# Kernel optimization log

Hardware: AMD Instinct MI355X
Metric: run time of the kernel (lower is better)

The kernel has to match this reference:

```python
import jax, jax.numpy as jnp
import numpy as np

E = 1024
H = 16
CH = E // H

def setup_inputs() -> dict:
    key = jax.random.key(0)
    ks = jax.random.split(key, 9)
    s = E ** -0.5
    return {
        'x': jax.random.normal(ks[0], (4, 2048, E), dtype=jnp.float32),
        'Wq': jax.random.normal(ks[1], (E, E), dtype=jnp.float32) * s,
        'bq': jnp.zeros((E,), dtype=jnp.float32),
        'Wk': jax.random.normal(ks[2], (E, E), dtype=jnp.float32) * s,
        'bk': jnp.zeros((E,), dtype=jnp.float32),
        'Wv': jax.random.normal(ks[3], (E, E), dtype=jnp.float32) * s,
        'bv': jnp.zeros((E,), dtype=jnp.float32),
        'Wo': jax.random.normal(ks[4], (E, E), dtype=jnp.float32) * s,
        'bo': jnp.zeros((E,), dtype=jnp.float32),
    }

def _split_heads(t):
    # [..., n, H*ch] -> [..., H, n, ch]
    b, n, e = t.shape
    return t.reshape(b, n, H, CH).transpose(0, 2, 1, 3)

def reference(x, Wq, bq, Wk, bk, Wv, bv, Wo, bo):
    scale = CH ** -0.5
    q = _split_heads(x @ Wq.T + bq)  # [b,H,n,ch]
    k = _split_heads(x @ Wk.T + bk)
    v = _split_heads(x @ Wv.T + bv)
    att = jnp.einsum('bhqc,bhkc->bhqk', q, k) * scale
    att = jax.nn.softmax(att, axis=-1)
    out = jnp.einsum('bhqk,bhkc->bhqc', att, v)  # [b,H,n,ch]
    b, h, n, c = out.shape
    out = out.transpose(0, 2, 1, 3).reshape(b, n, h * c)
    return out @ Wo.T + bo
```

## Files before the change

kernel.cpp:

```cpp
#include <hip/hip_runtime.h>
#include <stdint.h>

#define EMB   1024
#define NHEAD 16
#define CHD   64
#define NB    4
#define SEQ   2048
#define NTOK  (NB * SEQ)
#define KDIM  1024

typedef __attribute__((ext_vector_type(8))) short  bf16x8;
typedef __attribute__((ext_vector_type(4))) short  short4v;
typedef __attribute__((ext_vector_type(4))) float  f32x4;
typedef __attribute__((ext_vector_type(4))) float  float4v;

__device__ __forceinline__ short f2bf(float f) {
    unsigned int u = __float_as_uint(f);
    u += 0x7fffu + ((u >> 16) & 1u);
    return (short)(u >> 16);
}

__device__ __forceinline__ void async16(const short* g, short* l) {
    __builtin_amdgcn_global_load_lds((__attribute__((address_space(1))) void const*)g,
                                     (__attribute__((address_space(3))) void*)l, 16, 0, 0);
}

__global__ __launch_bounds__(256) void cvt_all(const float* __restrict__ x,
                                               const float* __restrict__ Wq,
                                               const float* __restrict__ Wk,
                                               const float* __restrict__ Wv,
                                               const float* __restrict__ Wo,
                                               short* __restrict__ xb,
                                               short* __restrict__ Wqb,
                                               short* __restrict__ Wkb,
                                               short* __restrict__ Wvb,
                                               short* __restrict__ Wob) {
    int bid = blockIdx.x;
    const float* src;
    short* dst;
    int idx;
    if (bid < 8192) {
        src = x; dst = xb; idx = bid * 256 + threadIdx.x;
    } else {
        int w  = (bid - 8192) >> 10;
        int lb = (bid - 8192) & 1023;
        src = (w == 0) ? Wq : (w == 1) ? Wk : (w == 2) ? Wv : Wo;
        dst = (w == 0) ? Wqb : (w == 1) ? Wkb : (w == 2) ? Wvb : Wob;
        idx = lb * 256 + threadIdx.x;
    }
    float4v v = ((const float4v*)src)[idx];
    short4v s;
    s.x = f2bf(v.x); s.y = f2bf(v.y); s.z = f2bf(v.z); s.w = f2bf(v.w);
    ((short4v*)dst)[idx] = s;
}

__device__ __forceinline__ void gemm_core(const short* __restrict__ Atile,
                                          const short* __restrict__ Btile,
                                          short* As, short* Bs, f32x4 acc[4][4]) {
    const int tid  = threadIdx.x;
    const int wave = tid >> 6, lane = tid & 63;
    const int quad = lane >> 4, l16 = lane & 15;
    const int wm = (wave >> 1) * 64, wn = (wave & 1) * 64;
    const int srow = lane >> 2;
    const int scol = (lane & 3) * 8;

    for (int k0 = 0; k0 < KDIM; k0 += 32) {
        __syncthreads();
#pragma unroll
        for (int c = 0; c < 2; ++c) {
            int chunk = wave * 2 + c;
            int row = chunk * 16 + srow;
            async16(Atile + (size_t)row * KDIM + k0 + scol, As + chunk * 512);
            async16(Btile + (size_t)row * KDIM + k0 + scol, Bs + chunk * 512);
        }
        __syncthreads();
        bf16x8 af[4], bfr[4];
#pragma unroll
        for (int i = 0; i < 4; ++i)
            af[i] = *(const bf16x8*)&As[(wm + i * 16 + l16) * 32 + quad * 8];
#pragma unroll
        for (int j = 0; j < 4; ++j)
            bfr[j] = *(const bf16x8*)&Bs[(wn + j * 16 + l16) * 32 + quad * 8];
#pragma unroll
        for (int i = 0; i < 4; ++i)
#pragma unroll
            for (int j = 0; j < 4; ++j)
                acc[i][j] = __builtin_amdgcn_mfma_f32_16x16x32_bf16(af[i], bfr[j], acc[i][j], 0, 0, 0);
    }
}

#define QSCALE 0.1803368801111204f
__global__ __launch_bounds__(256) void qkv_gemm(const short* __restrict__ xb,
                                                const short* __restrict__ Wqb,
                                                const short* __restrict__ Wkb,
                                                const short* __restrict__ Wvb,
                                                const float* __restrict__ bq,
                                                const float* __restrict__ bk,
                                                const float* __restrict__ bv,
                                                short* __restrict__ Qb,
                                                short* __restrict__ Kb,
                                                short* __restrict__ Vtb) {
    __shared__ short As[128 * 32], Bs[128 * 32];
    const int bm = blockIdx.x, bn = blockIdx.y;
    const int which = bn >> 3;
    const int ew = (bn & 7) * 128;
    const short* W    = (which == 0) ? Wqb : (which == 1) ? Wkb : Wvb;
    const float* bias = (which == 0) ? bq  : (which == 1) ? bk  : bv;
    const float sc    = (which == 0) ? QSCALE : 1.0f;

    const short* Xt = xb + (size_t)bm * 128 * KDIM;
    const short* Wt = W + (size_t)ew * KDIM;
    const short* Ap = (which == 2) ? Wt : Xt;
    const short* Bp = (which == 2) ? Xt : Wt;

    f32x4 acc[4][4];
    const f32x4 z = {0.f, 0.f, 0.f, 0.f};
#pragma unroll
    for (int i = 0; i < 4; ++i)
#pragma unroll
        for (int j = 0; j < 4; ++j) acc[i][j] = z;

    gemm_core(Ap, Bp, As, Bs, acc);

    const int lane = threadIdx.x & 63, wave = threadIdx.x >> 6;
    const int quad = lane >> 4, l16 = lane & 15;
    const int wm = (wave >> 1) * 64, wn = (wave & 1) * 64;

    if (which == 2) {
#pragma unroll
        for (int i = 0; i < 4; ++i)
#pragma unroll
            for (int j = 0; j < 4; ++j)
#pragma unroll
                for (int r = 0; r < 4; ++r) {
                    int e = ew + wm + i * 16 + quad * 4 + r;
                    int token = bm * 128 + wn + j * 16 + l16;
                    int bb = token >> 11, nn = token & 2047;
                    int hh = e >> 6, cc = e & 63;
                    Vtb[(((size_t)bb * NHEAD + hh) * CHD + cc) * SEQ + nn] =
                        f2bf(acc[i][j][r] + bias[e]);
                }
    } else {
        short* dst = which ? Kb : Qb;
#pragma unroll
        for (int i = 0; i < 4; ++i)
#pragma unroll
            for (int j = 0; j < 4; ++j)
#pragma unroll
                for (int r = 0; r < 4; ++r) {
                    int token = bm * 128 + wm + i * 16 + quad * 4 + r;
                    int bb = token >> 11, nn = token & 2047;
                    int e = ew + wn + j * 16 + l16;
                    int hh = e >> 6, cc = e & 63;
                    dst[(((size_t)bb * NHEAD + hh) * SEQ + nn) * CHD + cc] =
                        f2bf((acc[i][j][r] + bias[e]) * sc);
                }
    }
}

__global__ __launch_bounds__(256, 4) void attn(const short* __restrict__ Qb,
                                               const short* __restrict__ Kb,
                                               const short* __restrict__ Vtb,
                                               short* __restrict__ AOb) {
    __shared__ short Ks[16 * 512];
    __shared__ short Vs[16 * 512];

    const int qt = blockIdx.x;
    const int bh = blockIdx.y;
    const int tid = threadIdx.x, wave = tid >> 6, lane = tid & 63;
    const int quad = lane >> 4, l16 = lane & 15;

    const short* Kg = Kb  + (size_t)bh * SEQ * CHD;
    const short* Vg = Vtb + (size_t)bh * CHD * SEQ;

    bf16x8 qf0[2], qf1[2];
#pragma unroll
    for (int g = 0; g < 2; ++g) {
        const short* Qg = Qb + ((size_t)bh * SEQ + qt * 128 + wave * 32 + g * 16 + l16) * CHD;
        qf0[g] = *(const bf16x8*)(Qg + quad * 8);
        qf1[g] = *(const bf16x8*)(Qg + 32 + quad * 8);
    }

    const int kr = lane >> 3, ku = (lane & 7) ^ kr;
    const int vr = lane >> 4, vu = (lane & 15) ^ (vr << 2);

    int koff[4], voff[4];
#pragma unroll
    for (int cc = 0; cc < 4; ++cc) {
        int c = wave * 4 + cc;
        int l = c * 8 + kr;
        int j = l >> 4, m = l & 15;
        int kvg = ((j >> 1) << 5) + ((m >> 2) << 3) + ((j & 1) << 2) + (m & 3);
        koff[cc] = kvg * CHD + ku * 8;
        voff[cc] = (c * 4 + vr) * SEQ + vu * 8;
    }

    const int krow = l16 & 7;
    const int kbase = ((l16 >> 3) * 512) + krow * 64;
    const short* kp0 = Ks + kbase + ((quad ^ krow) << 3);
    const short* kp1 = Ks + kbase + (((4 + quad) ^ krow) << 3);
    const int vrow = l16 & 3;
    const short* vp = Vs + (l16 >> 2) * 512 + vrow * 128 + quad * 8;

    const f32x4 zf = {0.f, 0.f, 0.f, 0.f};
    const bf16x8 onesv = {16256, 16256, 16256, 16256, 16256, 16256, 16256, 16256};
    f32x4 O[2][4];
#pragma unroll
    for (int g = 0; g < 2; ++g)
#pragma unroll
        for (int nb = 0; nb < 4; ++nb) O[g][nb] = zf;
    f32x4 lacc[2];
    lacc[0] = zf; lacc[1] = zf;

    const short* Kgp = Kg;
    const short* Vgp = Vg;

    for (int kt = 0; kt < 16; ++kt) {
        __syncthreads();
#pragma unroll
        for (int cc = 0; cc < 4; ++cc) {
            int c = wave * 4 + cc;
            async16(Kgp + koff[cc], Ks + c * 512);
            async16(Vgp + voff[cc], Vs + c * 512);
        }
        Kgp += 128 * CHD;
        Vgp += 128;
        __syncthreads();

#pragma unroll
        for (int kk = 0; kk < 4; ++kk) {
            bf16x8 kA0 = *(const bf16x8*)(kp0 + (2 * kk) * 1024);
            bf16x8 kA1 = *(const bf16x8*)(kp1 + (2 * kk) * 1024);
            bf16x8 kB0 = *(const bf16x8*)(kp0 + (2 * kk + 1) * 1024);
            bf16x8 kB1 = *(const bf16x8*)(kp1 + (2 * kk + 1) * 1024);

            union { int i[4]; bf16x8 v; } pf[2];
#pragma unroll
            for (int g = 0; g < 2; ++g) {
                f32x4 sA = __builtin_amdgcn_mfma_f32_16x16x32_bf16(kA0, qf0[g], zf, 0, 0, 0);
                sA = __builtin_amdgcn_mfma_f32_16x16x32_bf16(kA1, qf1[g], sA, 0, 0, 0);
                f32x4 sB = __builtin_amdgcn_mfma_f32_16x16x32_bf16(kB0, qf0[g], zf, 0, 0, 0);
                sB = __builtin_amdgcn_mfma_f32_16x16x32_bf16(kB1, qf1[g], sB, 0, 0, 0);

                unsigned a0 = __float_as_uint(__builtin_amdgcn_exp2f(sA.x));
                unsigned a1 = __float_as_uint(__builtin_amdgcn_exp2f(sA.y));
                unsigned a2 = __float_as_uint(__builtin_amdgcn_exp2f(sA.z));
                unsigned a3 = __float_as_uint(__builtin_amdgcn_exp2f(sA.w));
                unsigned b0 = __float_as_uint(__builtin_amdgcn_exp2f(sB.x));
                unsigned b1 = __float_as_uint(__builtin_amdgcn_exp2f(sB.y));
                unsigned b2 = __float_as_uint(__builtin_amdgcn_exp2f(sB.z));
                unsigned b3 = __float_as_uint(__builtin_amdgcn_exp2f(sB.w));
                pf[g].i[0] = __builtin_amdgcn_perm(a1, a0, 0x07060302u);
                pf[g].i[1] = __builtin_amdgcn_perm(a3, a2, 0x07060302u);
                pf[g].i[2] = __builtin_amdgcn_perm(b1, b0, 0x07060302u);
                pf[g].i[3] = __builtin_amdgcn_perm(b3, b2, 0x07060302u);

                lacc[g] = __builtin_amdgcn_mfma_f32_16x16x32_bf16(pf[g].v, onesv, lacc[g], 0, 0, 0);
            }

            const short* vpk = vp + ((kk ^ vrow) << 5);
#pragma unroll
            for (int nb = 0; nb < 4; ++nb) {
                bf16x8 vf = *(const bf16x8*)(vpk + nb * 2048);
#pragma unroll
                for (int g = 0; g < 2; ++g)
                    O[g][nb] = __builtin_amdgcn_mfma_f32_16x16x32_bf16(pf[g].v, vf, O[g][nb], 0, 0, 0);
            }
        }
    }

    const int b = bh >> 4, h = bh & 15;
#pragma unroll
    for (int g = 0; g < 2; ++g) {
        float linv[4];
#pragma unroll
        for (int r = 0; r < 4; ++r) linv[r] = 1.0f / lacc[g][r];
#pragma unroll
        for (int nb = 0; nb < 4; ++nb)
#pragma unroll
            for (int r = 0; r < 4; ++r) {
                int n = qt * 128 + wave * 32 + g * 16 + quad * 4 + r;
                int cc = nb * 16 + l16;
                AOb[((size_t)b * SEQ + n) * EMB + h * CHD + cc] = f2bf(O[g][nb][r] * linv[r]);
            }
    }
}

__global__ __launch_bounds__(256) void out_gemm(const short* __restrict__ AOb,
                                                const short* __restrict__ Wob,
                                                const float* __restrict__ bo,
                                                float* __restrict__ out) {
    __shared__ short As[128 * 32], Bs[128 * 32];
    const int bm = blockIdx.x, bn = blockIdx.y;

    f32x4 acc[4][4];
    const f32x4 z = {0.f, 0.f, 0.f, 0.f};
#pragma unroll
    for (int i = 0; i < 4; ++i)
#pragma unroll
        for (int j = 0; j < 4; ++j) acc[i][j] = z;

    gemm_core(AOb + (size_t)bm * 128 * KDIM, Wob + (size_t)bn * 128 * KDIM, As, Bs, acc);

    const int lane = threadIdx.x & 63, wave = threadIdx.x >> 6;
    const int quad = lane >> 4, l16 = lane & 15;
    const int wm = (wave >> 1) * 64, wn = (wave & 1) * 64;
#pragma unroll
    for (int i = 0; i < 4; ++i)
#pragma unroll
        for (int j = 0; j < 4; ++j)
#pragma unroll
            for (int r = 0; r < 4; ++r) {
                int token = bm * 128 + wm + i * 16 + quad * 4 + r;
                int e = bn * 128 + wn + j * 16 + l16;
                out[(size_t)token * EMB + e] = acc[i][j][r] + bo[e];
            }
}

extern "C" void kernel_launch(void* const* d_in, const int* in_sizes, int n_in,
                              void* d_out, int out_size, void* d_ws, size_t ws_size,
                              hipStream_t stream) {
    const float* x  = (const float*)d_in[0];
    const float* Wq = (const float*)d_in[1];
    const float* bq = (const float*)d_in[2];
    const float* Wk = (const float*)d_in[3];
    const float* bk = (const float*)d_in[4];
    const float* Wv = (const float*)d_in[5];
    const float* bv = (const float*)d_in[6];
    const float* Wo = (const float*)d_in[7];
    const float* bo = (const float*)d_in[8];

    char* ws = (char*)d_ws;
    short* xb  = (short*)(ws + 0);
    short* Wqb = (short*)(ws + (size_t)16 * 1024 * 1024);
    short* Wkb = (short*)(ws + (size_t)18 * 1024 * 1024);
    short* Wvb = (short*)(ws + (size_t)20 * 1024 * 1024);
    short* Wob = (short*)(ws + (size_t)22 * 1024 * 1024);
    short* Qb  = (short*)(ws + (size_t)24 * 1024 * 1024);
    short* Kb  = (short*)(ws + (size_t)40 * 1024 * 1024);
    short* Vtb = (short*)(ws + (size_t)56 * 1024 * 1024);
    short* AOb = (short*)(ws + (size_t)72 * 1024 * 1024);

    cvt_all<<<dim3(8192 + 4096), dim3(256), 0, stream>>>(x, Wq, Wk, Wv, Wo,
                                                         xb, Wqb, Wkb, Wvb, Wob);
    qkv_gemm<<<dim3(64, 24), dim3(256), 0, stream>>>(xb, Wqb, Wkb, Wvb, bq, bk, bv, Qb, Kb, Vtb);
    attn<<<dim3(16, 64), dim3(256), 0, stream>>>(Qb, Kb, Vtb, AOb);
    out_gemm<<<dim3(64, 8), dim3(256), 0, stream>>>(AOb, Wob, bo, (float*)d_out);
}
```

Before: 281.8 us.

## Split QKV projection into pipelined 256x256 Q/K GEMM and separate V kernel

Replaces the combined QKV GEMM with a new 512-thread 256x256-tile GEMM for Q and K, and a separate V projection kernel. The Q/K kernel double-buffers LDS with async global-to-LDS loads, uses XOR-swizzled LDS layout, interleaves MFMA windows with barriers and setprio, and waits on explicit vmcnt. It relies on Wkb sitting directly after Wqb in the workspace so both can be read as one contiguous weight matrix. The goal is higher MFMA utilisation and more data reuse for the bulk of the projection, at the cost of 128KB of dynamic LDS per block and an extra kernel launch.

Result: faster. 262.3 us (-6.9%).

```diff
diff --git a/kernel.cpp b/kernel.cpp
--- a/kernel.cpp
+++ b/kernel.cpp
@@ -90,28 +90,149 @@
 }
 
 #define QSCALE 0.1803368801111204f
-__global__ __launch_bounds__(256) void qkv_gemm(const short* __restrict__ xb,
-                                                const short* __restrict__ Wqb,
-                                                const short* __restrict__ Wkb,
-                                                const short* __restrict__ Wvb,
+
+
+#define MFMA16(A,B,C) __builtin_amdgcn_mfma_f32_16x16x32_bf16(A,B,C,0,0,0)
+#define BARR  { __builtin_amdgcn_s_barrier(); __builtin_amdgcn_sched_barrier(0); }
+#define VMC4  asm volatile("s_waitcnt vmcnt(4)" ::: "memory");
+#define VMC0  asm volatile("s_waitcnt vmcnt(0)" ::: "memory");
+#define PRIO1 __builtin_amdgcn_s_setprio(1);
+#define PRIO0 __builtin_amdgcn_s_setprio(0);
+
+#define STAGE_A_(BUF,H,T) { \
+    async16(aS0 + (size_t)(H)*131072 + (T)*64, sm + (BUF)*32768 + (H)*8192 + stA); \
+    async16(aS1 + (size_t)(H)*131072 + (T)*64, sm + (BUF)*32768 + (H)*8192 + 4096 + stA); }
+#define STAGE_B_(BUF,H,T) { \
+    async16(bS0 + (size_t)(H)*131072 + (T)*64, sm + (BUF)*32768 + 16384 + (H)*8192 + stA); \
+    async16(bS1 + (size_t)(H)*131072 + (T)*64, sm + (BUF)*32768 + 16384 + (H)*8192 + 4096 + stA); }
+
+#define LDB_(BUF) { \
+    const short* _pb = sm + (BUF)*32768 + bro; \
+    bfr[0][0] = *(const bf16x8*)(_pb + ac0);        bfr[0][1] = *(const bf16x8*)(_pb + ac1); \
+    bfr[1][0] = *(const bf16x8*)(_pb + 1024 + ac0); bfr[1][1] = *(const bf16x8*)(_pb + 1024 + ac1); \
+    bfr[2][0] = *(const bf16x8*)(_pb + 2048 + ac0); bfr[2][1] = *(const bf16x8*)(_pb + 2048 + ac1); \
+    bfr[3][0] = *(const bf16x8*)(_pb + 3072 + ac0); bfr[3][1] = *(const bf16x8*)(_pb + 3072 + ac1); }
+
+#define LDA_(BUF,Q) { \
+    const short* _pa = sm + (BUF)*32768 + aro + (Q)*2048; \
+    af[0][0] = *(const bf16x8*)(_pa + ac0);        af[0][1] = *(const bf16x8*)(_pa + ac1); \
+    af[1][0] = *(const bf16x8*)(_pa + 1024 + ac0); af[1][1] = *(const bf16x8*)(_pa + 1024 + ac1); }
+
+#define MF_(Q) { \
+    acc[2*(Q)][0]   = MFMA16(af[0][0], bfr[0][0], acc[2*(Q)][0]); \
+    acc[2*(Q)][0]   = MFMA16(af[0][1], bfr[0][1], acc[2*(Q)][0]); \
+    acc[2*(Q)][1]   = MFMA16(af[0][0], bfr[1][0], acc[2*(Q)][1]); \
+    acc[2*(Q)][1]   = MFMA16(af[0][1], bfr[1][1], acc[2*(Q)][1]); \
+    acc[2*(Q)][2]   = MFMA16(af[0][0], bfr[2][0], acc[2*(Q)][2]); \
+    acc[2*(Q)][2]   = MFMA16(af[0][1], bfr[2][1], acc[2*(Q)][2]); \
+    acc[2*(Q)][3]   = MFMA16(af[0][0], bfr[3][0], acc[2*(Q)][3]); \
+    acc[2*(Q)][3]   = MFMA16(af[0][1], bfr[3][1], acc[2*(Q)][3]); \
+    acc[2*(Q)+1][0] = MFMA16(af[1][0], bfr[0][0], acc[2*(Q)+1][0]); \
+    acc[2*(Q)+1][0] = MFMA16(af[1][1], bfr[0][1], acc[2*(Q)+1][0]); \
+    acc[2*(Q)+1][1] = MFMA16(af[1][0], bfr[1][0], acc[2*(Q)+1][1]); \
+    acc[2*(Q)+1][1] = MFMA16(af[1][1], bfr[1][1], acc[2*(Q)+1][1]); \
+    acc[2*(Q)+1][2] = MFMA16(af[1][0], bfr[2][0], acc[2*(Q)+1][2]); \
+    acc[2*(Q)+1][2] = MFMA16(af[1][1], bfr[2][1], acc[2*(Q)+1][2]); \
+    acc[2*(Q)+1][3] = MFMA16(af[1][0], bfr[3][0], acc[2*(Q)+1][3]); \
+    acc[2*(Q)+1][3] = MFMA16(af[1][1], bfr[3][1], acc[2*(Q)+1][3]); }
+
+#define WINDOW(RB, AB, TA, BB, TB) \
+    LDB_(RB) LDA_(RB,0) STAGE_A_(AB,0,TA) BARR \
+    PRIO1 MF_(0) PRIO0 BARR \
+    LDA_(RB,1) STAGE_A_(AB,1,TA) BARR \
+    PRIO1 MF_(1) PRIO0 BARR \
+    LDA_(RB,2) STAGE_B_(BB,0,TB) BARR \
+    PRIO1 MF_(2) PRIO0 BARR \
+    LDA_(RB,3) STAGE_B_(BB,1,TB) BARR \
+    PRIO1 MF_(3) PRIO0 VMC4 BARR
+
+__global__ __launch_bounds__(512, 2) void qk256(const short* __restrict__ xb,
+                                                const short* __restrict__ Wqk,
                                                 const float* __restrict__ bq,
                                                 const float* __restrict__ bk,
-                                                const float* __restrict__ bv,
                                                 short* __restrict__ Qb,
-                                                short* __restrict__ Kb,
-                                                short* __restrict__ Vtb) {
+                                                short* __restrict__ Kb) {
+    extern __shared__ short sm[];
+    const int bm = blockIdx.x, bn = blockIdx.y;
+    const int tid = threadIdx.x;
+    const int w = tid >> 6, lane = tid & 63;
+    const int kq = lane >> 4, l16 = lane & 15;
+    const int wmi = w >> 2, wni = w & 3;
+
+    const int colsw = ((lane & 7) * 8) ^ (((lane >> 5) & 1) << 4);
+    const short* aS0 = xb  + (size_t)(bm * 256 + w * 8 + (lane >> 3)) * 1024 + colsw;
+    const short* aS1 = aS0 + (size_t)64 * 1024;
+    const short* bS0 = Wqk + (size_t)(bn * 256 + w * 8 + (lane >> 3)) * 1024 + colsw;
+    const short* bS1 = bS0 + (size_t)64 * 1024;
+    const int stA = w * 512;
+
+    const int swz = (l16 & 4) ? 16 : 0;
+    const int ac0 = (kq * 8) ^ swz;
+    const int ac1 = (32 + kq * 8) ^ swz;
+    const int aro = wmi * 8192 + l16 * 64;
+    const int bro = 16384 + (wni >> 1) * 8192 + ((wni & 1) * 64 + l16) * 64;
+
+    f32x4 acc[8][4];
+    const f32x4 z = {0.f, 0.f, 0.f, 0.f};
+#pragma unroll
+    for (int m = 0; m < 8; ++m)
+#pragma unroll
+        for (int n = 0; n < 4; ++n) acc[m][n] = z;
+    bf16x8 bfr[4][2], af[2][2];
+
+    STAGE_A_(0,0,0) STAGE_A_(0,1,0) STAGE_B_(0,0,0) STAGE_B_(0,1,0)
+    STAGE_B_(1,0,1) STAGE_B_(1,1,1)
+    VMC4 BARR
+
+    for (int it = 0; it < 7; ++it) {
+        const int te = 2 * it;
+        WINDOW(0, 1, te + 1, 0, te + 2)
+        WINDOW(1, 0, te + 2, 1, te + 3)
+    }
+    LDB_(0) LDA_(0,0) STAGE_A_(1,0,15) BARR
+    PRIO1 MF_(0) PRIO0 BARR
+    LDA_(0,1) STAGE_A_(1,1,15) BARR
+    PRIO1 MF_(1) PRIO0 BARR
+    LDA_(0,2) BARR
+    PRIO1 MF_(2) PRIO0 BARR
+    LDA_(0,3) BARR
+    PRIO1 MF_(3) PRIO0 VMC0 BARR
+    LDB_(1)
+    LDA_(1,0) MF_(0)
+    LDA_(1,1) MF_(1)
+    LDA_(1,2) MF_(2)
+    LDA_(1,3) MF_(3)
+
+    const bool isQ = (bn < 4);
+    const float* bias = isQ ? bq : bk;
+    short* dst = isQ ? Qb : Kb;
+    const float sc = isQ ? QSCALE : 1.0f;
+    const int fb = (bn & 3) * 256 + wni * 64 + l16;
+    const int tok0 = bm * 256 + wmi * 128 + kq * 4;
+#pragma unroll
+    for (int n = 0; n < 4; ++n) {
+        const int e = fb + n * 16;
+        const int hh = e >> 6, cc = e & 63;
+        const float bv_ = bias[e];
+#pragma unroll
+        for (int m = 0; m < 8; ++m)
+#pragma unroll
+            for (int r = 0; r < 4; ++r) {
+                const int tok = tok0 + m * 16 + r;
+                const int bb = tok >> 11, nn = tok & 2047;
+                dst[(((size_t)bb * NHEAD + hh) * SEQ + nn) * CHD + cc] =
+                    f2bf((acc[m][n][r] + bv_) * sc);
+            }
+    }
+}
+
+__global__ __launch_bounds__(256) void vproj(const short* __restrict__ xb,
+                                             const short* __restrict__ Wvb,
+                                             const float* __restrict__ bv,
+                                             short* __restrict__ Vtb) {
     __shared__ short As[128 * 32], Bs[128 * 32];
-    const int bm = blockIdx.x, bn = blockIdx.y;
-    const int which = bn >> 3;
-    const int ew = (bn & 7) * 128;
-    const short* W    = (which == 0) ? Wqb : (which == 1) ? Wkb : Wvb;
-    const float* bias = (which == 0) ? bq  : (which == 1) ? bk  : bv;
-    const float sc    = (which == 0) ? QSCALE : 1.0f;
-
-    const short* Xt = xb + (size_t)bm * 128 * KDIM;
-    const short* Wt = W + (size_t)ew * KDIM;
-    const short* Ap = (which == 2) ? Wt : Xt;
-    const short* Bp = (which == 2) ? Xt : Wt;
+    const int bm = blockIdx.x;
+    const int ew = blockIdx.y * 128;
 
     f32x4 acc[4][4];
     const f32x4 z = {0.f, 0.f, 0.f, 0.f};
@@ -120,42 +241,24 @@
 #pragma unroll
         for (int j = 0; j < 4; ++j) acc[i][j] = z;
 
-    gemm_core(Ap, Bp, As, Bs, acc);
+    gemm_core(Wvb + (size_t)ew * KDIM, xb + (size_t)bm * 128 * KDIM, As, Bs, acc);
 
     const int lane = threadIdx.x & 63, wave = threadIdx.x >> 6;
     const int quad = lane >> 4, l16 = lane & 15;
     const int wm = (wave >> 1) * 64, wn = (wave & 1) * 64;
-
-    if (which == 2) {
-#pragma unroll
-        for (int i = 0; i < 4; ++i)
-#pragma unroll
-            for (int j = 0; j < 4; ++j)
-#pragma unroll
-                for (int r = 0; r < 4; ++r) {
-                    int e = ew + wm + i * 16 + quad * 4 + r;
-                    int token = bm * 128 + wn + j * 16 + l16;
-                    int bb = token >> 11, nn = token & 2047;
-                    int hh = e >> 6, cc = e & 63;
-                    Vtb[(((size_t)bb * NHEAD + hh) * CHD + cc) * SEQ + nn] =
-                        f2bf(acc[i][j][r] + bias[e]);
-                }
-    } else {
-        short* dst = which ? Kb : Qb;
-#pragma unroll
-        for (int i = 0; i < 4; ++i)
-#pragma unroll
-            for (int j = 0; j < 4; ++j)
-#pragma unroll
-                for (int r = 0; r < 4; ++r) {
-                    int token = bm * 128 + wm + i * 16 + quad * 4 + r;
-                    int bb = token >> 11, nn = token & 2047;
-                    int e = ew + wn + j * 16 + l16;
-                    int hh = e >> 6, cc = e & 63;
-                    dst[(((size_t)bb * NHEAD + hh) * SEQ + nn) * CHD + cc] =
-                        f2bf((acc[i][j][r] + bias[e]) * sc);
-                }
-    }
+#pragma unroll
+    for (int i = 0; i < 4; ++i)
+#pragma unroll
+        for (int j = 0; j < 4; ++j)
+#pragma unroll
+            for (int r = 0; r < 4; ++r) {
+                int e = ew + wm + i * 16 + quad * 4 + r;
+                int token = bm * 128 + wn + j * 16 + l16;
+                int bb = token >> 11, nn = token & 2047;
+                int hh = e >> 6, cc = e & 63;
+                Vtb[(((size_t)bb * NHEAD + hh) * CHD + cc) * SEQ + nn] =
+                    f2bf(acc[i][j][r] + bv[e]);
+            }
 }
 
 __global__ __launch_bounds__(256, 4) void attn(const short* __restrict__ Qb,
@@ -341,9 +444,17 @@
     short* Vtb = (short*)(ws + (size_t)56 * 1024 * 1024);
     short* AOb = (short*)(ws + (size_t)72 * 1024 * 1024);
 
+    static bool s_cfg = false;
+    if (!s_cfg) {
+        hipFuncSetAttribute(reinterpret_cast<const void*>(qk256),
+                            hipFuncAttributeMaxDynamicSharedMemorySize, 131072);
+        s_cfg = true;
+    }
+
     cvt_all<<<dim3(8192 + 4096), dim3(256), 0, stream>>>(x, Wq, Wk, Wv, Wo,
                                                          xb, Wqb, Wkb, Wvb, Wob);
-    qkv_gemm<<<dim3(64, 24), dim3(256), 0, stream>>>(xb, Wqb, Wkb, Wvb, bq, bk, bv, Qb, Kb, Vtb);
+    qk256<<<dim3(32, 8), dim3(512), 131072, stream>>>(xb, Wqb, bq, bk, Qb, Kb);
+    vproj<<<dim3(64, 8), dim3(256), 0, stream>>>(xb, Wvb, bv, Vtb);
     attn<<<dim3(16, 64), dim3(256), 0, stream>>>(Qb, Kb, Vtb, AOb);
     out_gemm<<<dim3(64, 8), dim3(256), 0, stream>>>(AOb, Wob, bo, (float*)d_out);
 }
```
